# Kernel tuning notes

Hardware: AMD Instinct MI355X
Metric: run time of the kernel (lower is better)

## Reference

```python
import jax, jax.numpy as jnp
import numpy as np
from jax import lax

NPOINT = 512
RADIUS = 0.2
NSAMPLE = 32
BN_EPS = 1e-5


def farthest_point_sample(xyz, npoint):
    # xyz: [B, N, 3] -> centroids: [B, npoint] int32
    # Deterministic init (index 0) instead of torch's randint for reproducibility.
    B, N, _ = xyz.shape
    batch = jnp.arange(B)

    def body(carry, _):
        distance, farthest = carry
        centroid = xyz[batch, farthest][:, None, :]          # [B,1,3]
        dist = jnp.sum((xyz - centroid) ** 2, -1)             # [B,N]
        distance = jnp.minimum(distance, dist)
        new_far = jnp.argmax(distance, axis=-1).astype(jnp.int32)
        return (distance, new_far), farthest

    init = (jnp.full((B, N), 1e10, xyz.dtype), jnp.zeros((B,), jnp.int32))
    _, cents = lax.scan(body, init, None, length=npoint)      # [npoint, B]
    return cents.T


def gather_points(points, idx):
    # points: [B,N,C], idx: [B,...] -> [B,...,C]
    return jax.vmap(lambda p, i: p[i])(points, idx)


def query_ball_point(radius, nsample, xyz, new_xyz):
    # xyz: [B,N,3], new_xyz: [B,S,3] -> idx: [B,S,nsample]
    B, N, _ = xyz.shape
    sqrdists = jnp.sum((new_xyz[:, :, None, :] - xyz[:, None, :, :]) ** 2, -1)  # [B,S,N]
    gidx = jnp.where(sqrdists > radius * radius, N, jnp.arange(N))
    gidx = jnp.sort(gidx, axis=-1)[:, :, :nsample]
    first = gidx[:, :, :1]
    return jnp.where(gidx == N, first, gidx)


def setup_inputs() -> dict:
    key = jax.random.key(0)
    ks = jax.random.split(key, 8)
    B, N, D = 16, 8192, 3
    inp = {
        "xyz": jax.random.uniform(ks[0], (B, N, 3), jnp.float32),
        "points": jax.random.normal(ks[1], (B, N, D), jnp.float32),
    }
    chans = [D + 3, 64, 64, 128]
    for i in range(3):
        cin, cout = chans[i], chans[i + 1]
        inp[f"w{i}"] = jax.random.normal(ks[2 + i], (cout, cin), jnp.float32) / np.sqrt(cin)
        inp[f"b{i}"] = jnp.zeros((cout,), jnp.float32)
        inp[f"g{i}"] = jnp.ones((cout,), jnp.float32)
        inp[f"beta{i}"] = jnp.zeros((cout,), jnp.float32)
    return inp


def _forward(xyz, points, params):
    fps_idx = farthest_point_sample(xyz, NPOINT)               # [B,S]
    new_xyz = gather_points(xyz, fps_idx)                      # [B,S,3]
    idx = query_ball_point(RADIUS, NSAMPLE, xyz, new_xyz)      # [B,S,K]
    grouped_xyz = gather_points(xyz, idx) - new_xyz[:, :, None, :]  # [B,S,K,3]
    grouped_pts = gather_points(points, idx)                   # [B,S,K,D]
    feat = jnp.concatenate([grouped_xyz, grouped_pts], -1)     # [B,S,K,3+D]
    for w, b, g, be in params:
        feat = jnp.einsum('bskc,oc->bsko', feat, w) + b        # 1x1 conv
        mean = jnp.mean(feat, axis=(0, 1, 2))                  # BN (training stats)
        var = jnp.var(feat, axis=(0, 1, 2))
        feat = g * (feat - mean) * lax.rsqrt(var + BN_EPS) + be
        feat = jax.nn.relu(feat)
    new_points = jnp.max(feat, axis=2)                         # max over nsample -> [B,S,Cout]
    return new_xyz, new_points


def reference(xyz, points, w0, b0, g0, beta0, w1, b1, g1, beta1, w2, b2, g2, beta2):
    params = [(w0, b0, g0, beta0), (w1, b1, g1, beta1), (w2, b2, g2, beta2)]
    return _forward(xyz, points, params)
```

## Files before the change

kernel.cpp:

```cpp
#include <hip/hip_runtime.h>
#include <hip/hip_bf16.h>
#include <cstdint>
#include <cstddef>

#define NB 16
#define NN 8192
#define NS 512
#define NK 32
#define NG (NB*NS)
#define GPB 4
#define NBLK (NG/GPB)
#define NPOSI 262144
#define SBLK 16

__device__ __forceinline__ double sq3d(double dx, double dy, double dz){
#pragma clang fp contract(off)
  const double a = dx*dx;
  const double b = dy*dy;
  const double c = dz*dz;
  return (a + b) + c;
}

template<int CTRL>
__device__ __forceinline__ unsigned dpp_umax_step(unsigned v){
  const unsigned o = (unsigned)__builtin_amdgcn_update_dpp(0, (int)v, CTRL, 0xf, 0xf, false);
  return v > o ? v : o;
}
__device__ __forceinline__ unsigned wave_umax63(unsigned v){
  v = dpp_umax_step<0xB1>(v);
  v = dpp_umax_step<0x4E>(v);
  v = dpp_umax_step<0x141>(v);
  v = dpp_umax_step<0x140>(v);
  v = dpp_umax_step<0x142>(v);
  v = dpp_umax_step<0x143>(v);
  return v;
}
__device__ __forceinline__ unsigned grp16_umax(unsigned v){
  v = dpp_umax_step<0xB1>(v);
  v = dpp_umax_step<0x4E>(v);
  v = dpp_umax_step<0x141>(v);
  v = dpp_umax_step<0x140>(v);
  return v;
}

__device__ __forceinline__ unsigned mort4(unsigned v){
  return (v & 1u) | ((v & 2u) << 2) | ((v & 4u) << 4) | ((v & 8u) << 6);
}

__global__ __launch_bounds__(1024) void k_morton(const float* __restrict__ xyz,
                                                 int* __restrict__ ord){
  const int b = blockIdx.x;
  const int t = threadIdx.x;
  const float* __restrict__ X = xyz + (size_t)b*NN*3;
  __shared__ unsigned sHist[4096];
  __shared__ unsigned sWT[16];
  for (int k=t; k<4096; k+=1024) sHist[k] = 0u;
  __syncthreads();
  unsigned code[8];
#pragma unroll
  for (int j=0;j<8;++j){
    const int p = t + 1024*j;
    const float x=X[p*3+0], y=X[p*3+1], z=X[p*3+2];
    const unsigned ix=(unsigned)min(15,max(0,(int)(x*16.f)));
    const unsigned iy=(unsigned)min(15,max(0,(int)(y*16.f)));
    const unsigned iz=(unsigned)min(15,max(0,(int)(z*16.f)));
    code[j] = mort4(ix) | (mort4(iy)<<1) | (mort4(iz)<<2);
    atomicAdd(&sHist[code[j]], 1u);
  }
  __syncthreads();
  {
    const uint4 h = ((const uint4*)sHist)[t];
    const unsigned l1=h.x, l2=h.x+h.y, l3=h.x+h.y+h.z, tot=l3+h.w;
    unsigned inc = tot;
    const int lane = t & 63;
#pragma unroll
    for (int d2=1; d2<64; d2<<=1){
      const unsigned v = __shfl_up(inc, d2);
      if (lane >= d2) inc += v;
    }
    const unsigned wexc = inc - tot;
    if (lane == 63) sWT[t>>6] = inc;
    __syncthreads();
    if (t == 0){
      unsigned run = 0;
#pragma unroll
      for (int k=0;k<16;++k){ const unsigned v=sWT[k]; sWT[k]=run; run+=v; }
    }
    __syncthreads();
    const unsigned base = sWT[t>>6] + wexc;
    uint4 o; o.x=base; o.y=base+l1; o.z=base+l2; o.w=base+l3;
    ((uint4*)sHist)[t] = o;
  }
  __syncthreads();
#pragma unroll
  for (int j=0;j<8;++j){
    const unsigned pos = atomicAdd(&sHist[code[j]], 1u);
    ord[(size_t)b*NN + pos] = t + 1024*j;
  }
}

__global__ __launch_bounds__(1024) void k_fps(const float* __restrict__ xyz,
                                              const int* __restrict__ ord,
                                              float* __restrict__ newxyz){
  const int b = blockIdx.x;
  const int t = threadIdx.x;
  const float* __restrict__ X = xyz + (size_t)b*NN*3;

  __shared__ float4 sP[NN];
  __shared__ unsigned long long sW0[2][16];
  __shared__ unsigned long long sWv64[2][16];

  int oidx[8];
#pragma unroll
  for (int j=0;j<8;++j){
    const int p = t + 1024*j;
    sP[p] = make_float4(X[p*3+0], X[p*3+1], X[p*3+2], 0.f);
    oidx[j] = ord[(size_t)b*NN + 8*t + j];
  }
  if (t < 16){ sW0[0][t]=0ull; sW0[1][t]=0ull; }
  __syncthreads();

  float px[8], py[8], pz[8], thr[8];
  double dd[8];
#pragma unroll
  for (int j=0;j<8;++j){
    const float4 q = sP[oidx[j]];
    px[j]=q.x; py[j]=q.y; pz[j]=q.z;
    dd[j]=1e10;
    thr[j]=fmaf(1e10f, 0x1p-19f, 1e10f);
  }
  float ctx=0.f, cty=0.f, ctz=0.f;
#pragma unroll
  for (int j=0;j<8;++j){ ctx+=px[j]; cty+=py[j]; ctz+=pz[j]; }
  ctx*=0.125f; cty*=0.125f; ctz*=0.125f;
  float r2m = 0.f;
#pragma unroll
  for (int j=0;j<8;++j){
    const float ax=px[j]-ctx, ay=py[j]-cty, az=pz[j]-ctz;
    r2m = fmaxf(r2m, fmaf(az,az,fmaf(ay,ay,ax*ax)));
  }
  const float rT = sqrtf(r2m)*(1.0f+0x1p-18f) + 0x1p-20f;

  double tmax = 1e10;
  float  tmax32 = 1e10f;
  int tio = oidx[0], ts = 0;
#pragma unroll
  for (int j=1;j<8;++j) if (oidx[j] < tio){ tio = oidx[j]; ts = j; }
  float skipgate = tmax32*(1.0f+0x1p-14f);

  int f = 0;
  const int lane = t & 63, wid = t >> 6;

  for (int i=0;i<NS-1;++i){
    const int par = i & 1;
    const float4 cf = sP[f];
    const float cx=cf.x, cy=cf.y, cz=cf.z;
    if (t == 0){
      float* o = newxyz + ((size_t)b*NS + i)*3;
      o[0]=cx; o[1]=cy; o[2]=cz;
    }

    const float bx=cx-ctx, by=cy-cty, bz=cz-ctz;
    const float ddc = fmaf(bz,bz,fmaf(by,by,bx*bx));
    const float dcc = sqrtf(ddc);
    float s = dcc - rT; s = s - dcc*0x1p-16f;
    const bool engage = !(s > 0.f && s*s >= skipgate);

    if (engage){
      float e[8]; float mmin = 1e30f;
#pragma unroll
      for (int j=0;j<8;++j){
        const float ax=px[j]-cx, ay=py[j]-cy, az=pz[j]-cz;
        const float d32 = fmaf(az, az, fmaf(ay, ay, ax*ax));
        e[j] = d32 - thr[j];
        mmin = fminf(mmin, e[j]);
      }
      if (__builtin_expect(mmin <= 0.f, 0)){
        const double cxd=(double)cx, cyd=(double)cy, czd=(double)cz;
        bool needscan = false;
#pragma unroll
        for (int j=0;j<8;++j){
          if (e[j] <= 0.f){
            const double d64 = sq3d((double)px[j]-cxd, (double)py[j]-cyd, (double)pz[j]-czd);
            const double nd = fmin(dd[j], d64);
            needscan |= (j == ts) | (nd == tmax);
            dd[j] = nd;
            const float nd32 = (float)nd;
            thr[j] = fmaf(nd32, 0x1p-19f, nd32);
          }
        }
        if (needscan){
          double tm = dd[0]; int io = oidx[0]; int s0 = 0;
#pragma unroll
          for (int j=1;j<8;++j)
            if (dd[j] > tm || (dd[j] == tm && oidx[j] < io)){ tm=dd[j]; io=oidx[j]; s0=j; }
          tmax=tm; tio=io; ts=s0; tmax32=(float)tm;
          skipgate = tmax32*(1.0f+0x1p-14f);
        }
      }
    }

    const unsigned myb = __float_as_uint(tmax32);
    const unsigned wm = (unsigned)__builtin_amdgcn_readlane((int)wave_umax63(myb), 63);
    const unsigned long long mask = __ballot(myb == wm);
    int writer;
    if (__builtin_expect(__popcll(mask) == 1, 1)){
      writer = (int)__builtin_ctzll(mask);
    } else {
      double bestv = -1.0; int bestid = 0x7fffffff;
      unsigned long long mm = mask;
      while (mm){
        const int l = (int)__builtin_ctzll(mm);
        const double v = __shfl(tmax, l);
        const int   id = __shfl(tio, l);
        if (v > bestv || (v == bestv && id < bestid)){ bestv=v; bestid=id; }
        mm &= mm - 1;
      }
      writer = (int)__builtin_ctzll(__ballot(tmax == bestv && tio == bestid));
    }
    if (lane == writer){
      sWv64[par][wid] = (unsigned long long)__double_as_longlong(tmax);
      const unsigned long long pk = ((unsigned long long)wm << 32)
                                  | ((unsigned long long)(unsigned)(i+1) << 13)
                                  | (unsigned long long)(unsigned)tio;
      __hip_atomic_store(&sW0[par][wid], pk,
                         __ATOMIC_RELEASE, __HIP_MEMORY_SCOPE_WORKGROUP);
    }

    const unsigned want = (unsigned)(i+1);
    unsigned long long w;
    do {
      w = __hip_atomic_load(&sW0[par][lane & 15],
                            __ATOMIC_RELAXED, __HIP_MEMORY_SCOPE_WORKGROUP);
    } while (__ballot((((unsigned)w >> 13) & 1023u) == want) != ~0ull);
    __builtin_amdgcn_fence(__ATOMIC_ACQUIRE, "workgroup");

    const unsigned wf   = (unsigned)(w >> 32);
    const unsigned idxw = (unsigned)w & 8191u;
    const unsigned m32  = grp16_umax(wf);
    const unsigned long long cm = __ballot(wf == m32);
    if (__builtin_expect(__popcll(cm) == 4, 1)){
      f = __shfl((int)idxw, (int)__builtin_ctzll(cm));
    } else {
      unsigned long long mm = cm & 0xFFFFull;
      double bv = -1.0; int bid = 0x7fffffff;
      while (mm){
        const int l = (int)__builtin_ctzll(mm);
        const double v = __longlong_as_double((long long)sWv64[par][l]);
        const int   id = __shfl((int)idxw, l);
        if (v > bv || (v == bv && id < bid)){ bv = v; bid = id; }
        mm &= mm - 1;
      }
      f = bid;
    }
  }
  if (t == 0){
    const float4 cf = sP[f];
    float* o = newxyz + ((size_t)b*NS + (NS-1))*3;
    o[0]=cf.x; o[1]=cf.y; o[2]=cf.z;
  }
}

__global__ __launch_bounds__(256) void k_ball(const float* __restrict__ xyz,
                                              const float* __restrict__ newxyz,
                                              int* __restrict__ idx){
  const int w = (blockIdx.x << 2) + (threadIdx.x >> 6);
  const int lane = threadIdx.x & 63;
  const int b = w >> 9;
  const float* __restrict__ C = newxyz + (size_t)w*3;
  const float cxf=C[0], cyf=C[1], czf=C[2];
  const double cx=(double)cxf, cy=(double)cyf, cz=(double)czf;
  const float* __restrict__ X = xyz + (size_t)b*NN*3;
  int* __restrict__ out = idx + (size_t)w*NK;
  const double R2 = 0.2*0.2;
  const float r2lo = 0.04f*(1.0f - 0x1p-16f);
  const float r2hi = 0.04f*(1.0f + 0x1p-16f);
  int count = 0, first = 0;
  for (int base=0; base<NN && count<NK; base+=64){
    const int p = base + lane;
    const float ax=X[p*3+0]-cxf, ay=X[p*3+1]-cyf, az=X[p*3+2]-czf;
    const float d32 = fmaf(az, az, fmaf(ay, ay, ax*ax));
    bool q;
    if (d32 <= r2lo)      q = true;
    else if (d32 > r2hi)  q = false;
    else {
      const double d = sq3d((double)X[p*3+0]-cx, (double)X[p*3+1]-cy, (double)X[p*3+2]-cz);
      q = !(d > R2);
    }
    const unsigned long long m = __ballot(q);
    if (q){
      const int pos = count + __popcll(m & ((1ull<<lane)-1ull));
      if (pos < NK) out[pos] = p;
    }
    if (count == 0 && m) first = base + __builtin_ctzll(m);
    count += __popcll(m);
  }
  if (lane >= count && lane < NK) out[lane] = first;
}

__device__ __forceinline__ void stats_reduce(
    float v[4][8], float* __restrict__ sRed, int t, int tp, int tc, int blk,
    int chtot, int choff, bool domm,
    float* __restrict__ pS, float* __restrict__ pQ,
    float* __restrict__ mxp, float* __restrict__ mnp)
{
  __syncthreads();
  float S=0.f, Q=0.f;
  for (int m=0;m<4;++m){
#pragma unroll
    for (int i=0;i<8;++i) sRed[tp*68 + tc*8 + i] = v[m][i];
    __syncthreads();
    if (t < 64){
      float mxv = -3.402823466e38f, mnv = 3.402823466e38f;
#pragma unroll
      for (int j=0;j<32;++j){
        const float x = sRed[j*68 + t];
        S += x; Q += x*x;
        mxv = fmaxf(mxv,x); mnv = fminf(mnv,x);
      }
      if (domm){
        const int gg = blk*GPB + m;
        mxp[(size_t)gg*128 + choff + t] = mxv;
        mnp[(size_t)gg*128 + choff + t] = mnv;
      }
    }
    __syncthreads();
  }
  if (t < 64){
    pS[(size_t)blk*chtot + choff + t] = S;
    pQ[(size_t)blk*chtot + choff + t] = Q;
  }
}

__device__ __forceinline__ void mm64(const float* __restrict__ sXl,
                                     const float* __restrict__ sWl,
                                     int tp, int tc, float v[4][8]){
#pragma unroll 4
  for (int k=0;k<64;++k){
    float xv[4], wv[8];
#pragma unroll
    for (int m=0;m<4;++m) xv[m] = sXl[(tp+32*m)*65 + k];
#pragma unroll
    for (int i=0;i<8;++i) wv[i] = sWl[(tc*8+i)*65 + k];
#pragma unroll
    for (int m=0;m<4;++m)
#pragma unroll
      for (int i=0;i<8;++i) v[m][i] += xv[m]*wv[i];
  }
}

template<int DEPTH>
__global__ __launch_bounds__(256) void k_pass(
    const float* __restrict__ xyz, const float* __restrict__ points,
    const float* __restrict__ newxyz, const int* __restrict__ idx,
    const float* __restrict__ w0, const float* __restrict__ b0,
    const float* __restrict__ w1, const float* __restrict__ b1,
    const float* __restrict__ w2, const float* __restrict__ b2,
    const float* __restrict__ ac,
    float* __restrict__ pS, float* __restrict__ pQ,
    float* __restrict__ mxp, float* __restrict__ mnp)
{
  __shared__ float smem[(DEPTH>=1) ? 14784 : 2304];
  float* sX0 = smem;
  float* sW0 = smem + 1024;
  float* sV  = smem + 1600;
  float* sRed= smem;
  float* sB2 = smem + 2176;
  float* sW1 = smem + 2304;
  float* sX  = smem + 6464;

  const int t = threadIdx.x;
  const int blk = blockIdx.x;
  const int tc = t & 7, tp = t >> 3;

  for (int i=t;i<384;i+=256) sW0[(i/6)*9 + (i%6)] = w0[i];
  if (t < 64) sV[t] = b0[t];
  if constexpr (DEPTH >= 1){
    if (t < 64){ sV[64+t]=ac[t]; sV[128+t]=ac[64+t]; sV[192+t]=b1[t]; }
    for (int i=t;i<4096;i+=256) sW1[(i>>6)*65 + (i&63)] = w1[i];
  }
  if constexpr (DEPTH == 2){
    if (t < 64){ sV[256+t]=ac[128+t]; sV[320+t]=ac[192+t]; }
    if (t < 128) sB2[t] = b2[t];
  }

  {
    const int pos = t & 127;
    const int gg = blk*GPB + (pos >> 5);
    const int b  = gg >> 9;
    const int id = idx[gg*NK + (pos & 31)];
    if (t < 128){
      const float* __restrict__ P = xyz + ((size_t)b*NN + id)*3;
      const float* __restrict__ C = newxyz + (size_t)gg*3;
      sX0[pos*8+0] = P[0]-C[0];
      sX0[pos*8+1] = P[1]-C[1];
      sX0[pos*8+2] = P[2]-C[2];
    } else {
      const float* __restrict__ P = points + ((size_t)b*NN + id)*3;
      sX0[pos*8+3] = P[0];
      sX0[pos*8+4] = P[1];
      sX0[pos*8+5] = P[2];
    }
  }
  __syncthreads();

  float v[4][8];
#pragma unroll
  for (int m=0;m<4;++m){
    const int pos = tp + 32*m;
    float xr[6];
#pragma unroll
    for (int c=0;c<6;++c) xr[c] = sX0[pos*8+c];
#pragma unroll
    for (int i=0;i<8;++i){
      const int ch = tc*8+i;
      float acc = sV[ch];
#pragma unroll
      for (int c=0;c<6;++c) acc += sW0[ch*9+c]*xr[c];
      v[m][i] = acc;
    }
  }

  if constexpr (DEPTH == 0){
    stats_reduce(v, sRed, t, tp, tc, blk, 64, 0, false, pS, pQ, mxp, mnp);
    return;
  } else {
#pragma unroll
    for (int m=0;m<4;++m){
      const int pos = tp + 32*m;
#pragma unroll
      for (int i=0;i<8;++i){
        const int ch = tc*8+i;
        sX[pos*65+ch] = fmaxf(sV[64+ch]*v[m][i] + sV[128+ch], 0.f);
      }
    }
    __syncthreads();
#pragma unroll
    for (int m=0;m<4;++m)
#pragma unroll
      for (int i=0;i<8;++i) v[m][i] = sV[192 + tc*8 + i];
    mm64(sX, sW1, tp, tc, v);

    if constexpr (DEPTH == 1){
      stats_reduce(v, sRed, t, tp, tc, blk, 64, 0, false, pS, pQ, mxp, mnp);
      return;
    } else {
      __syncthreads();
#pragma unroll
      for (int m=0;m<4;++m){
        const int pos = tp + 32*m;
#pragma unroll
        for (int i=0;i<8;++i){
          const int ch = tc*8+i;
          sX[pos*65+ch] = fmaxf(sV[256+ch]*v[m][i] + sV[320+ch], 0.f);
        }
      }
      __syncthreads();
      for (int o=0;o<2;++o){
        for (int i=t;i<4096;i+=256) sW1[(i>>6)*65 + (i&63)] = w2[o*4096 + i];
        __syncthreads();
#pragma unroll
        for (int m=0;m<4;++m)
#pragma unroll
          for (int i=0;i<8;++i) v[m][i] = sB2[o*64 + tc*8 + i];
        mm64(sX, sW1, tp, tc, v);
        stats_reduce(v, sRed, t, tp, tc, blk, 128, o*64, true, pS, pQ, mxp, mnp);
      }
      return;
    }
  }
}

__global__ __launch_bounds__(1024) void k_stats1(const float* __restrict__ pS,
                                                 const float* __restrict__ pQ,
                                                 float* __restrict__ pP, int CH){
  __shared__ float sS[1024], sQ[1024];
  const int t = threadIdx.x, blk = blockIdx.x;
  const int ch = t & (CH-1);
  const int seg = t / CH;
  const int SEG = 1024 / CH;
  const int rows = (NBLK/SBLK) / SEG;
  const int j0 = blk*(NBLK/SBLK) + seg*rows;
  float S=0.f, Q=0.f;
#pragma unroll 4
  for (int r=0;r<rows;++r){
    const size_t o = (size_t)(j0+r)*CH + ch;
    S += pS[o]; Q += pQ[o];
  }
  sS[t]=S; sQ[t]=Q;
  __syncthreads();
  if (t < CH){
    float aS=0.f, aQ=0.f;
    for (int s2=0;s2<SEG;++s2){ aS += sS[s2*CH+ch]; aQ += sQ[s2*CH+ch]; }
    pP[(size_t)blk*2*CH + ch]      = aS;
    pP[(size_t)blk*2*CH + CH + ch] = aQ;
  }
}

__global__ __launch_bounds__(128) void k_stats2(const float* __restrict__ pP,
                                                const float* __restrict__ g,
                                                const float* __restrict__ beta,
                                                float* __restrict__ a, float* __restrict__ c,
                                                int CH){
  const int ch = threadIdx.x;
  if (ch >= CH) return;
  float S=0.f, Q=0.f;
#pragma unroll
  for (int k=0;k<SBLK;++k){
    S += pP[(size_t)k*2*CH + ch];
    Q += pP[(size_t)k*2*CH + CH + ch];
  }
  const float mean = S * (1.f/(float)NPOSI);
  const float var  = fmaxf(Q * (1.f/(float)NPOSI) - mean*mean, 0.f);
  const float av = g[ch] * rsqrtf(var + 1e-5f);
  a[ch] = av;
  c[ch] = beta[ch] - mean*av;
}

__global__ __launch_bounds__(256) void k_final(const float* __restrict__ mxp, const float* __restrict__ mnp,
                                               const float* __restrict__ a, const float* __restrict__ c,
                                               float* __restrict__ out){
  const int i = blockIdx.x*256 + threadIdx.x;
  const int ch = i & 127;
  const float av = a[ch], cv = c[ch];
  const float vv = (av >= 0.f) ? mxp[i] : mnp[i];
  out[i] = fmaxf(av*vv + cv, 0.f);
}

extern "C" void kernel_launch(void* const* d_in, const int* in_sizes, int n_in,
                              void* d_out, int out_size, void* d_ws, size_t ws_size,
                              hipStream_t stream){
  (void)in_sizes; (void)n_in; (void)out_size;
  const float* xyz    = (const float*)d_in[0];
  const float* points = (const float*)d_in[1];
  const float* w0 = (const float*)d_in[2];
  const float* b0 = (const float*)d_in[3];
  const float* g0 = (const float*)d_in[4];
  const float* be0= (const float*)d_in[5];
  const float* w1 = (const float*)d_in[6];
  const float* b1 = (const float*)d_in[7];
  const float* g1 = (const float*)d_in[8];
  const float* be1= (const float*)d_in[9];
  const float* w2 = (const float*)d_in[10];
  const float* b2 = (const float*)d_in[11];
  const float* g2 = (const float*)d_in[12];
  const float* be2= (const float*)d_in[13];

  float* out_newxyz = (float*)d_out;
  float* out_newpts = out_newxyz + (size_t)NB*NS*3;

  char* ws = (char*)d_ws;
  int*   idx = (int*)ws;
  float* ac  = (float*)(ws + (1u<<20));
  float* pS  = (float*)(ws + (1u<<20) + 4096);
  float* pQ  = pS + (size_t)NBLK*128;
  float* mxp = pQ + (size_t)NBLK*128;
  float* mnp = mxp + (size_t)NG*128;
  float* pP  = mnp + (size_t)NG*128;
  const size_t need = (1u<<20) + 4096 + (size_t)2*NBLK*128*4 + (size_t)2*NG*128*4
                    + (size_t)SBLK*2*128*4;
  if (ws_size < need) return;

  int* ord = idx;

  k_morton<<<NB, 1024, 0, stream>>>(xyz, ord);
  k_fps  <<<NB, 1024, 0, stream>>>(xyz, ord, out_newxyz);
  k_ball <<<NG/4, 256, 0, stream>>>(xyz, out_newxyz, idx);

  k_pass<0><<<NBLK,256,0,stream>>>(xyz,points,out_newxyz,idx,w0,b0,w1,b1,w2,b2,ac,pS,pQ,mxp,mnp);
  k_stats1<<<SBLK,1024,0,stream>>>(pS,pQ,pP,64);
  k_stats2<<<1,128,0,stream>>>(pP,g0,be0, ac+0,   ac+64,  64);
  k_pass<1><<<NBLK,256,0,stream>>>(xyz,points,out_newxyz,idx,w0,b0,w1,b1,w2,b2,ac,pS,pQ,mxp,mnp);
  k_stats1<<<SBLK,1024,0,stream>>>(pS,pQ,pP,64);
  k_stats2<<<1,128,0,stream>>>(pP,g1,be1, ac+128, ac+192, 64);
  k_pass<2><<<NBLK,256,0,stream>>>(xyz,points,out_newxyz,idx,w0,b0,w1,b1,w2,b2,ac,pS,pQ,mxp,mnp);
  k_stats1<<<SBLK,1024,0,stream>>>(pS,pQ,pP,128);
  k_stats2<<<1,128,0,stream>>>(pP,g2,be2, ac+256, ac+384, 128);
  k_final<<<(NG*128)/256,256,0,stream>>>(mxp,mnp,ac+256,ac+384,out_newpts);
}
```

Measured before the change: 1.030 ms.

## Cache layer-1 pre-BN activations in bf16 to skip recompute in pass 2

Adds a pass that computes layer 0 and layer 1 once and stores the pre-BN layer-1 outputs as packed bf16 in workspace. A second kernel reads them back, applies BN1 and ReLU, and runs the layer-2 matmul, so the final pass no longer recomputes the gather, layer 0 and layer 1. The cost is an extra 32 MB write plus read, and bf16 rounding of intermediate activations, which may shift BN statistics and outputs slightly. It only runs when the workspace is large enough, with the old path kept as a fallback.

```diff
diff --git a/kernel.cpp b/kernel.cpp
--- a/kernel.cpp
+++ b/kernel.cpp
@@ -46,6 +46,15 @@
 __device__ __forceinline__ unsigned mort4(unsigned v){
   return (v & 1u) | ((v & 2u) << 2) | ((v & 4u) << 4) | ((v & 8u) << 6);
 }
+
+__device__ __forceinline__ unsigned bf2pk(float lo, float hi){
+  unsigned a=__float_as_uint(lo), b=__float_as_uint(hi);
+  a = (a + 0x7fffu + ((a>>16)&1u)) >> 16;
+  b = (b + 0x7fffu + ((b>>16)&1u)) >> 16;
+  return (b<<16) | a;
+}
+__device__ __forceinline__ float bflo(unsigned u){ return __uint_as_float(u<<16); }
+__device__ __forceinline__ float bfhi(unsigned u){ return __uint_as_float(u & 0xffff0000u); }
 
 __global__ __launch_bounds__(1024) void k_morton(const float* __restrict__ xyz,
                                                  int* __restrict__ ord){
@@ -471,6 +480,153 @@
   }
 }
 
+__global__ __launch_bounds__(256) void k_pass1s(
+    const float* __restrict__ xyz, const float* __restrict__ points,
+    const float* __restrict__ newxyz, const int* __restrict__ idx,
+    const float* __restrict__ w0, const float* __restrict__ b0,
+    const float* __restrict__ w1, const float* __restrict__ b1,
+    const float* __restrict__ ac, unsigned* __restrict__ y1c,
+    float* __restrict__ pS, float* __restrict__ pQ,
+    float* __restrict__ mxp, float* __restrict__ mnp)
+{
+  __shared__ float smem[14784];
+  float* sX0 = smem;
+  float* sW0 = smem + 1024;
+  float* sV  = smem + 1600;
+  float* sRed= smem;
+  float* sW1 = smem + 2304;
+  float* sX  = smem + 6464;
+
+  const int t = threadIdx.x;
+  const int blk = blockIdx.x;
+  const int tc = t & 7, tp = t >> 3;
+
+  for (int i=t;i<384;i+=256) sW0[(i/6)*9 + (i%6)] = w0[i];
+  if (t < 64){ sV[t]=b0[t]; sV[64+t]=ac[t]; sV[128+t]=ac[64+t]; sV[192+t]=b1[t]; }
+  for (int i=t;i<4096;i+=256) sW1[(i>>6)*65 + (i&63)] = w1[i];
+
+  {
+    const int pos = t & 127;
+    const int gg = blk*GPB + (pos >> 5);
+    const int b  = gg >> 9;
+    const int id = idx[gg*NK + (pos & 31)];
+    if (t < 128){
+      const float* __restrict__ P = xyz + ((size_t)b*NN + id)*3;
+      const float* __restrict__ C = newxyz + (size_t)gg*3;
+      sX0[pos*8+0] = P[0]-C[0];
+      sX0[pos*8+1] = P[1]-C[1];
+      sX0[pos*8+2] = P[2]-C[2];
+    } else {
+      const float* __restrict__ P = points + ((size_t)b*NN + id)*3;
+      sX0[pos*8+3] = P[0];
+      sX0[pos*8+4] = P[1];
+      sX0[pos*8+5] = P[2];
+    }
+  }
+  __syncthreads();
+
+  float v[4][8];
+#pragma unroll
+  for (int m=0;m<4;++m){
+    const int pos = tp + 32*m;
+    float xr[6];
+#pragma unroll
+    for (int c=0;c<6;++c) xr[c] = sX0[pos*8+c];
+#pragma unroll
+    for (int i=0;i<8;++i){
+      const int ch = tc*8+i;
+      float acc = sV[ch];
+#pragma unroll
+      for (int c=0;c<6;++c) acc += sW0[ch*9+c]*xr[c];
+      v[m][i] = acc;
+    }
+  }
+#pragma unroll
+  for (int m=0;m<4;++m){
+    const int pos = tp + 32*m;
+#pragma unroll
+    for (int i=0;i<8;++i){
+      const int ch = tc*8+i;
+      sX[pos*65+ch] = fmaxf(sV[64+ch]*v[m][i] + sV[128+ch], 0.f);
+    }
+  }
+  __syncthreads();
+#pragma unroll
+  for (int m=0;m<4;++m)
+#pragma unroll
+    for (int i=0;i<8;++i) v[m][i] = sV[192 + tc*8 + i];
+  mm64(sX, sW1, tp, tc, v);
+
+#pragma unroll
+  for (int m=0;m<4;++m){
+    const int pos = tp + 32*m;
+    uint4 pk;
+    pk.x = bf2pk(v[m][0], v[m][1]);
+    pk.y = bf2pk(v[m][2], v[m][3]);
+    pk.z = bf2pk(v[m][4], v[m][5]);
+    pk.w = bf2pk(v[m][6], v[m][7]);
+    ((uint4*)y1c)[((size_t)blk*128 + pos)*8 + tc] = pk;
+  }
+
+  stats_reduce(v, sRed, t, tp, tc, blk, 64, 0, false, pS, pQ, mxp, mnp);
+}
+
+__global__ __launch_bounds__(256) void k_pass2l(
+    const unsigned* __restrict__ y1c,
+    const float* __restrict__ w2, const float* __restrict__ b2,
+    const float* __restrict__ ac,
+    float* __restrict__ pS, float* __restrict__ pQ,
+    float* __restrict__ mxp, float* __restrict__ mnp)
+{
+  __shared__ float smem[14784];
+  float* sV  = smem + 1600;
+  float* sRed= smem;
+  float* sB2 = smem + 2176;
+  float* sW1 = smem + 2304;
+  float* sX  = smem + 6464;
+
+  const int t = threadIdx.x;
+  const int blk = blockIdx.x;
+  const int tc = t & 7, tp = t >> 3;
+
+  if (t < 64){ sV[t]=ac[128+t]; sV[64+t]=ac[192+t]; }
+  if (t < 128) sB2[t] = b2[t];
+
+  float v[4][8];
+#pragma unroll
+  for (int m=0;m<4;++m){
+    const int pos = tp + 32*m;
+    const uint4 pk = ((const uint4*)y1c)[((size_t)blk*128 + pos)*8 + tc];
+    v[m][0]=bflo(pk.x); v[m][1]=bfhi(pk.x);
+    v[m][2]=bflo(pk.y); v[m][3]=bfhi(pk.y);
+    v[m][4]=bflo(pk.z); v[m][5]=bfhi(pk.z);
+    v[m][6]=bflo(pk.w); v[m][7]=bfhi(pk.w);
+  }
+  __syncthreads();
+
+#pragma unroll
+  for (int m=0;m<4;++m){
+    const int pos = tp + 32*m;
+#pragma unroll
+    for (int i=0;i<8;++i){
+      const int ch = tc*8+i;
+      sX[pos*65+ch] = fmaxf(sV[ch]*v[m][i] + sV[64+ch], 0.f);
+    }
+  }
+  __syncthreads();
+
+  for (int o=0;o<2;++o){
+    for (int i2=t;i2<4096;i2+=256) sW1[(i2>>6)*65 + (i2&63)] = w2[o*4096 + i2];
+    __syncthreads();
+#pragma unroll
+    for (int m=0;m<4;++m)
+#pragma unroll
+      for (int i=0;i<8;++i) v[m][i] = sB2[o*64 + tc*8 + i];
+    mm64(sX, sW1, tp, tc, v);
+    stats_reduce(v, sRed, t, tp, tc, blk, 128, o*64, true, pS, pQ, mxp, mnp);
+  }
+}
+
 __global__ __launch_bounds__(1024) void k_stats1(const float* __restrict__ pS,
                                                  const float* __restrict__ pQ,
                                                  float* __restrict__ pP, int CH){
@@ -557,9 +713,12 @@
   float* mxp = pQ + (size_t)NBLK*128;
   float* mnp = mxp + (size_t)NG*128;
   float* pP  = mnp + (size_t)NG*128;
-  const size_t need = (1u<<20) + 4096 + (size_t)2*NBLK*128*4 + (size_t)2*NG*128*4
-                    + (size_t)SBLK*2*128*4;
-  if (ws_size < need) return;
+  unsigned* y1c = (unsigned*)(pP + (size_t)SBLK*2*128);
+  const size_t need_small = (1u<<20) + 4096 + (size_t)2*NBLK*128*4 + (size_t)2*NG*128*4
+                          + (size_t)SBLK*2*128*4;
+  const size_t need_big   = need_small + (size_t)NPOSI*64*2;
+  if (ws_size < need_small) return;
+  const bool big = (ws_size >= need_big);
 
   int* ord = idx;
 
@@ -570,10 +729,17 @@
   k_pass<0><<<NBLK,256,0,stream>>>(xyz,points,out_newxyz,idx,w0,b0,w1,b1,w2,b2,ac,pS,pQ,mxp,mnp);
   k_stats1<<<SBLK,1024,0,stream>>>(pS,pQ,pP,64);
   k_stats2<<<1,128,0,stream>>>(pP,g0,be0, ac+0,   ac+64,  64);
-  k_pass<1><<<NBLK,256,0,stream>>>(xyz,points,out_newxyz,idx,w0,b0,w1,b1,w2,b2,ac,pS,pQ,mxp,mnp);
-  k_stats1<<<SBLK,1024,0,stream>>>(pS,pQ,pP,64);
-  k_stats2<<<1,128,0,stream>>>(pP,g1,be1, ac+128, ac+192, 64);
-  k_pass<2><<<NBLK,256,0,stream>>>(xyz,points,out_newxyz,idx,w0,b0,w1,b1,w2,b2,ac,pS,pQ,mxp,mnp);
+  if (big){
+    k_pass1s<<<NBLK,256,0,stream>>>(xyz,points,out_newxyz,idx,w0,b0,w1,b1,ac,y1c,pS,pQ,mxp,mnp);
+    k_stats1<<<SBLK,1024,0,stream>>>(pS,pQ,pP,64);
+    k_stats2<<<1,128,0,stream>>>(pP,g1,be1, ac+128, ac+192, 64);
+    k_pass2l<<<NBLK,256,0,stream>>>(y1c,w2,b2,ac,pS,pQ,mxp,mnp);
+  } else {
+    k_pass<1><<<NBLK,256,0,stream>>>(xyz,points,out_newxyz,idx,w0,b0,w1,b1,w2,b2,ac,pS,pQ,mxp,mnp);
+    k_stats1<<<SBLK,1024,0,stream>>>(pS,pQ,pP,64);
+    k_stats2<<<1,128,0,stream>>>(pP,g1,be1, ac+128, ac+192, 64);
+    k_pass<2><<<NBLK,256,0,stream>>>(xyz,points,out_newxyz,idx,w0,b0,w1,b1,w2,b2,ac,pS,pQ,mxp,mnp);
+  }
   k_stats1<<<SBLK,1024,0,stream>>>(pS,pQ,pP,128);
   k_stats2<<<1,128,0,stream>>>(pP,g2,be2, ac+256, ac+384, 128);
   k_final<<<(NG*128)/256,256,0,stream>>>(mxp,mnp,ac+256,ac+384,out_newpts);
```

After: 1.011 ms. No clear change (-1.9%).
